# Kernel optimization log

Hardware: AMD Instinct MI355X
Metric: run time of the kernel (lower is better)

## Reference

```python
import jax, jax.numpy as jnp
import numpy as np

N, T, n, C, C2 = 4, 8, 16384, 64, 64

def setup_inputs() -> dict:
    key = jax.random.key(0)
    k1, k2, k3, k4, k5 = jax.random.split(key, 5)
    return {
        "key_mem": jax.random.normal(k1, (N, T, n, C), dtype=jnp.float32),
        "val_mem": jax.random.normal(k2, (N, T, n, C2), dtype=jnp.float32),
        "key_cur": jax.random.normal(k3, (N, n, C), dtype=jnp.float32),
        "val_cur": jax.random.normal(k4, (N, n, C2), dtype=jnp.float32),
        "alpha": jax.random.normal(k5, (1,), dtype=jnp.float32),
    }

def reference(key_mem, val_mem, key_cur, val_cur, alpha):
    # kv_mul: contract memory tokens (T*n) -> (N, C, C2), tiny matrix
    kv_mul = jnp.einsum('btnc,btnd->bcd', key_mem, val_mem)
    # softmax over the C axis (dim=1 in torch layout (N, C, C2))
    kv_mul = jax.nn.softmax(kv_mul, axis=1)
    # out: (N, n, C) @ (N, C, C2) -> (N, n, C2)
    out = jnp.einsum('bnc,bcd->bnd', key_cur, kv_mul)
    return alpha * out + val_cur
```

## Files before the change

kernel.cpp:

```cpp
#include <hip/hip_runtime.h>
#include <math.h>

#define T_DIM   8
#define N_TOK   16384
#define C_DIM   64
#define K_TOT   (T_DIM * N_TOK)
#define N_BATCH 4

__global__ __launch_bounds__(256, 2) void k1_accum(
    const float* __restrict__ key, const float* __restrict__ val,
    float* __restrict__ part, int bpb) {
  int blk  = blockIdx.x;
  int b    = blk / bpb;
  int p    = blk % bpb;
  int wave = threadIdx.x >> 6;
  int lane = threadIdx.x & 63;
  int i = lane >> 3;
  int j = lane & 7;

  int wpb   = bpb * 4;
  int q     = p * 4 + wave;
  int steps = K_TOT / wpb;

  float acc[8][8];
#pragma unroll
  for (int a = 0; a < 8; a++)
#pragma unroll
    for (int c = 0; c < 8; c++) acc[a][c] = 0.f;

  const float4* k4 = (const float4*)key;
  const float4* v4 = (const float4*)val;
  size_t base_row = (size_t)b * K_TOT;

  int k = q;
#pragma unroll 2
  for (int s = 0; s < steps; s++, k += wpb) {
    size_t row = (base_row + (size_t)k) * 16;
    float4 ka = k4[row + 2 * i];
    float4 kb = k4[row + 2 * i + 1];
    float4 va = v4[row + 2 * j];
    float4 vb = v4[row + 2 * j + 1];
    float kr[8] = {ka.x, ka.y, ka.z, ka.w, kb.x, kb.y, kb.z, kb.w};
    float vr[8] = {va.x, va.y, va.z, va.w, vb.x, vb.y, vb.z, vb.w};
#pragma unroll
    for (int a = 0; a < 8; a++)
#pragma unroll
      for (int c = 0; c < 8; c++)
        acc[a][c] = fmaf(kr[a], vr[c], acc[a][c]);
  }

  __shared__ float red[4][4096];
#pragma unroll
  for (int a = 0; a < 8; a++) {
    int c = 8 * i + a;
    *(float4*)&red[wave][c * 64 + 8 * j] =
        make_float4(acc[a][0], acc[a][1], acc[a][2], acc[a][3]);
    *(float4*)&red[wave][c * 64 + 8 * j + 4] =
        make_float4(acc[a][4], acc[a][5], acc[a][6], acc[a][7]);
  }
  __syncthreads();

  int t = threadIdx.x;
  float* dst = part + (size_t)blk * 4096;
#pragma unroll
  for (int x = 0; x < 16; x++) {
    int e = t + 256 * x;
    dst[e] = red[0][e] + red[1][e] + red[2][e] + red[3][e];
  }
}

__global__ __launch_bounds__(256, 4) void k2_reduce(
    const float* __restrict__ part, float* __restrict__ kv, int bpb) {
  int b  = blockIdx.x >> 6;
  int c  = blockIdx.x & 63;
  int p4 = threadIdx.x >> 6;
  int d  = threadIdx.x & 63;

  float s = 0.f;
  int iters = bpb >> 2;
  const float* src = part + (size_t)(b * bpb) * 4096 + c * 64 + d;
#pragma unroll 4
  for (int x = 0; x < iters; x++) s += src[(size_t)(p4 + 4 * x) * 4096];

  __shared__ float l[256];
  l[threadIdx.x] = s;
  __syncthreads();
  if (p4 == 0)
    kv[((size_t)b * 64 + c) * 64 + d] = l[d] + l[64 + d] + l[128 + d] + l[192 + d];
}

__global__ __launch_bounds__(64, 4) void k3_out(
    const float* __restrict__ kv, const float* __restrict__ keyc,
    const float* __restrict__ valc, const float* __restrict__ alphap,
    float* __restrict__ out) {
  __shared__ float kT[64 * 68];
  __shared__ float P[64 * 64];

  int bb = blockIdx.x >> 8;
  int mb = blockIdx.x & 255;
  int m0 = mb * 64;
  int lane = threadIdx.x;
  int i = lane >> 3;
  int j = lane & 7;

  const float* kvb = kv + (size_t)bb * 4096;
  float mx = -3.4e38f;
  for (int c = 0; c < 64; c++) {
    float v = kvb[c * 64 + lane];
    P[c * 64 + lane] = v;
    mx = fmaxf(mx, v);
  }
  float sum = 0.f;
  for (int c = 0; c < 64; c++) {
    float e = __expf(P[c * 64 + lane] - mx);
    P[c * 64 + lane] = e;
    sum += e;
  }
  float inv = 1.f / sum;
  for (int c = 0; c < 64; c++) P[c * 64 + lane] *= inv;

  const float* kbp = keyc + ((size_t)bb * N_TOK + m0) * 64;
#pragma unroll 4
  for (int r = 0; r < 64; r++) kT[lane * 68 + r] = kbp[(size_t)r * 64 + lane];
  __syncthreads();

  float acc[8][8];
#pragma unroll
  for (int a = 0; a < 8; a++)
#pragma unroll
    for (int d = 0; d < 8; d++) acc[a][d] = 0.f;

  for (int c = 0; c < 64; c++) {
    float4 a0 = *(const float4*)&kT[c * 68 + 8 * i];
    float4 a1 = *(const float4*)&kT[c * 68 + 8 * i + 4];
    float4 p0 = *(const float4*)&P[c * 64 + 8 * j];
    float4 p1 = *(const float4*)&P[c * 64 + 8 * j + 4];
    float ar[8] = {a0.x, a0.y, a0.z, a0.w, a1.x, a1.y, a1.z, a1.w};
    float pr[8] = {p0.x, p0.y, p0.z, p0.w, p1.x, p1.y, p1.z, p1.w};
#pragma unroll
    for (int a = 0; a < 8; a++)
#pragma unroll
      for (int d = 0; d < 8; d++)
        acc[a][d] = fmaf(ar[a], pr[d], acc[a][d]);
  }

  float alpha = alphap[0];
  size_t ob = ((size_t)bb * N_TOK + m0) * 64;
#pragma unroll
  for (int a = 0; a < 8; a++) {
    int m = 8 * i + a;
    size_t off = ob + (size_t)m * 64 + 8 * j;
    float4 v0 = *(const float4*)&valc[off];
    float4 v1 = *(const float4*)&valc[off + 4];
    float4 o0 = make_float4(fmaf(alpha, acc[a][0], v0.x),
                            fmaf(alpha, acc[a][1], v0.y),
                            fmaf(alpha, acc[a][2], v0.z),
                            fmaf(alpha, acc[a][3], v0.w));
    float4 o1 = make_float4(fmaf(alpha, acc[a][4], v1.x),
                            fmaf(alpha, acc[a][5], v1.y),
                            fmaf(alpha, acc[a][6], v1.z),
                            fmaf(alpha, acc[a][7], v1.w));
    *(float4*)&out[off] = o0;
    *(float4*)&out[off + 4] = o1;
  }
}

extern "C" void kernel_launch(void* const* d_in, const int* in_sizes, int n_in,
                              void* d_out, int out_size, void* d_ws,
                              size_t ws_size, hipStream_t stream) {
  const float* key_mem = (const float*)d_in[0];
  const float* val_mem = (const float*)d_in[1];
  const float* key_cur = (const float*)d_in[2];
  const float* val_cur = (const float*)d_in[3];
  const float* alpha   = (const float*)d_in[4];
  float* out = (float*)d_out;
  float* ws  = (float*)d_ws;

  int bpb = 128;
  while (bpb > 8 &&
         ((size_t)(4 * bpb) * 4096 + 4096 * N_BATCH) * sizeof(float) > ws_size)
    bpb >>= 2;

  float* part = ws;
  float* kv   = ws + (size_t)(4 * bpb) * 4096;

  k1_accum<<<4 * bpb, 256, 0, stream>>>(key_mem, val_mem, part, bpb);
  k2_reduce<<<256, 256, 0, stream>>>(part, kv, bpb);
  k3_out<<<N_BATCH * (N_TOK / 64), 64, 0, stream>>>(kv, key_cur, val_cur, alpha,
                                                    out);
}
```

Baseline: 353.9 us.

## Prefetch loads in accumulation, split softmax kernel, widen output kernel blocks

k1 now runs 512-thread blocks and software-prefetches the next row's key/value float4s while it accumulates the current outer product. Its cross-wave reduction moves to a staged shared-memory scheme with half the LDS footprint. Softmax moves out of the per-tile output kernel into a tiny separate kernel, so each of the 1024 output blocks no longer recomputes it. k3 uses 256 threads with coalesced key loads and a 2x8 register tile, which adds a launch and trades per-thread reuse for more parallelism.

```diff
diff --git a/kernel.cpp b/kernel.cpp
--- a/kernel.cpp
+++ b/kernel.cpp
@@ -7,7 +7,7 @@
 #define K_TOT   (T_DIM * N_TOK)
 #define N_BATCH 4
 
-__global__ __launch_bounds__(256, 2) void k1_accum(
+__global__ __launch_bounds__(512, 4) void k1_accum(
     const float* __restrict__ key, const float* __restrict__ val,
     float* __restrict__ part, int bpb) {
   int blk  = blockIdx.x;
@@ -18,8 +18,8 @@
   int i = lane >> 3;
   int j = lane & 7;
 
-  int wpb   = bpb * 4;
-  int q     = p * 4 + wave;
+  int wpb   = bpb * 8;
+  int q     = p * 8 + wave;
   int steps = K_TOT / wpb;
 
   float acc[8][8];
@@ -30,16 +30,34 @@
 
   const float4* k4 = (const float4*)key;
   const float4* v4 = (const float4*)val;
-  size_t base_row = (size_t)b * K_TOT;
-
-  int k = q;
+  size_t base = (size_t)b * K_TOT;
+
+  size_t row = (base + (size_t)q) * 16;
+  float4 ka = k4[row + 2 * i];
+  float4 kb = k4[row + 2 * i + 1];
+  float4 va = v4[row + 2 * j];
+  float4 vb = v4[row + 2 * j + 1];
+
+  int k = q + wpb;
 #pragma unroll 2
-  for (int s = 0; s < steps; s++, k += wpb) {
-    size_t row = (base_row + (size_t)k) * 16;
-    float4 ka = k4[row + 2 * i];
-    float4 kb = k4[row + 2 * i + 1];
-    float4 va = v4[row + 2 * j];
-    float4 vb = v4[row + 2 * j + 1];
+  for (int s = 0; s < steps - 1; s++, k += wpb) {
+    size_t r2 = (base + (size_t)k) * 16;
+    float4 nka = k4[r2 + 2 * i];
+    float4 nkb = k4[r2 + 2 * i + 1];
+    float4 nva = v4[r2 + 2 * j];
+    float4 nvb = v4[r2 + 2 * j + 1];
+    {
+      float kr[8] = {ka.x, ka.y, ka.z, ka.w, kb.x, kb.y, kb.z, kb.w};
+      float vr[8] = {va.x, va.y, va.z, va.w, vb.x, vb.y, vb.z, vb.w};
+#pragma unroll
+      for (int a = 0; a < 8; a++)
+#pragma unroll
+        for (int c = 0; c < 8; c++)
+          acc[a][c] = fmaf(kr[a], vr[c], acc[a][c]);
+    }
+    ka = nka; kb = nkb; va = nva; vb = nvb;
+  }
+  {
     float kr[8] = {ka.x, ka.y, ka.z, ka.w, kb.x, kb.y, kb.z, kb.w};
     float vr[8] = {va.x, va.y, va.z, va.w, vb.x, vb.y, vb.z, vb.w};
 #pragma unroll
@@ -49,23 +67,43 @@
         acc[a][c] = fmaf(kr[a], vr[c], acc[a][c]);
   }
 
-  __shared__ float red[4][4096];
-#pragma unroll
-  for (int a = 0; a < 8; a++) {
-    int c = 8 * i + a;
-    *(float4*)&red[wave][c * 64 + 8 * j] =
-        make_float4(acc[a][0], acc[a][1], acc[a][2], acc[a][3]);
-    *(float4*)&red[wave][c * 64 + 8 * j + 4] =
-        make_float4(acc[a][4], acc[a][5], acc[a][6], acc[a][7]);
+  __shared__ float red[2][4096];
+  if (wave < 2) {
+#pragma unroll
+    for (int a = 0; a < 8; a++) {
+      int c = 8 * i + a;
+      *(float4*)&red[wave][c * 64 + 8 * j] =
+          make_float4(acc[a][0], acc[a][1], acc[a][2], acc[a][3]);
+      *(float4*)&red[wave][c * 64 + 8 * j + 4] =
+          make_float4(acc[a][4], acc[a][5], acc[a][6], acc[a][7]);
+    }
   }
   __syncthreads();
-
+#pragma unroll
+  for (int g = 1; g < 4; g++) {
+    if (wave >= 2 * g && wave < 2 * g + 2) {
+      int wb = wave - 2 * g;
+#pragma unroll
+      for (int a = 0; a < 8; a++) {
+        int c = 8 * i + a;
+        float4* d0 = (float4*)&red[wb][c * 64 + 8 * j];
+        float4* d1 = (float4*)&red[wb][c * 64 + 8 * j + 4];
+        float4 x0 = *d0, x1 = *d1;
+        *d0 = make_float4(x0.x + acc[a][0], x0.y + acc[a][1],
+                          x0.z + acc[a][2], x0.w + acc[a][3]);
+        *d1 = make_float4(x1.x + acc[a][4], x1.y + acc[a][5],
+                          x1.z + acc[a][6], x1.w + acc[a][7]);
+      }
+    }
+    __syncthreads();
+  }
+
+  float* dst = part + (size_t)blk * 4096;
   int t = threadIdx.x;
-  float* dst = part + (size_t)blk * 4096;
-#pragma unroll
-  for (int x = 0; x < 16; x++) {
-    int e = t + 256 * x;
-    dst[e] = red[0][e] + red[1][e] + red[2][e] + red[3][e];
+#pragma unroll
+  for (int x = 0; x < 8; x++) {
+    int e = t + 512 * x;
+    dst[e] = red[0][e] + red[1][e];
   }
 }
 
@@ -89,67 +127,87 @@
     kv[((size_t)b * 64 + c) * 64 + d] = l[d] + l[64 + d] + l[128 + d] + l[192 + d];
 }
 
-__global__ __launch_bounds__(64, 4) void k3_out(
-    const float* __restrict__ kv, const float* __restrict__ keyc,
+__global__ __launch_bounds__(64, 1) void k2b_softmax(
+    const float* __restrict__ kv, float* __restrict__ P) {
+  int b = blockIdx.x;
+  int d = threadIdx.x;
+  const float* s = kv + (size_t)b * 4096 + d;
+  float v[64];
+#pragma unroll
+  for (int c = 0; c < 64; c++) v[c] = s[c * 64];
+  float mx = v[0];
+#pragma unroll
+  for (int c = 1; c < 64; c++) mx = fmaxf(mx, v[c]);
+  float sum = 0.f;
+#pragma unroll
+  for (int c = 0; c < 64; c++) {
+    v[c] = __expf(v[c] - mx);
+    sum += v[c];
+  }
+  float inv = 1.f / sum;
+  float* o = P + (size_t)b * 4096 + d;
+#pragma unroll
+  for (int c = 0; c < 64; c++) o[c * 64] = v[c] * inv;
+}
+
+__global__ __launch_bounds__(256, 4) void k3_out(
+    const float* __restrict__ P, const float* __restrict__ keyc,
     const float* __restrict__ valc, const float* __restrict__ alphap,
     float* __restrict__ out) {
+  __shared__ float Ps[4096];
   __shared__ float kT[64 * 68];
-  __shared__ float P[64 * 64];
 
   int bb = blockIdx.x >> 8;
   int mb = blockIdx.x & 255;
   int m0 = mb * 64;
-  int lane = threadIdx.x;
-  int i = lane >> 3;
-  int j = lane & 7;
-
-  const float* kvb = kv + (size_t)bb * 4096;
-  float mx = -3.4e38f;
+  int t = threadIdx.x;
+
+  const float4* p4 = (const float4*)(P + (size_t)bb * 4096);
+  float4* ps4 = (float4*)Ps;
+#pragma unroll
+  for (int u = 0; u < 4; u++) ps4[t + 256 * u] = p4[t + 256 * u];
+
+  int r  = t >> 2;
+  int cb = (t & 3) * 16;
+  const float* krow = keyc + ((size_t)bb * N_TOK + m0 + r) * 64;
+#pragma unroll
+  for (int u = 0; u < 4; u++) {
+    float4 kk = *(const float4*)&krow[cb + 4 * u];
+    int c = cb + 4 * u;
+    kT[(c + 0) * 68 + r] = kk.x;
+    kT[(c + 1) * 68 + r] = kk.y;
+    kT[(c + 2) * 68 + r] = kk.z;
+    kT[(c + 3) * 68 + r] = kk.w;
+  }
+  __syncthreads();
+
+  int wave = t >> 6, lane = t & 63;
+  int mi = lane >> 3, j = lane & 7;
+  int m = wave * 16 + mi * 2;
+
+  float acc[2][8];
+#pragma unroll
+  for (int a = 0; a < 2; a++)
+#pragma unroll
+    for (int d = 0; d < 8; d++) acc[a][d] = 0.f;
+
+#pragma unroll 4
   for (int c = 0; c < 64; c++) {
-    float v = kvb[c * 64 + lane];
-    P[c * 64 + lane] = v;
-    mx = fmaxf(mx, v);
-  }
-  float sum = 0.f;
-  for (int c = 0; c < 64; c++) {
-    float e = __expf(P[c * 64 + lane] - mx);
-    P[c * 64 + lane] = e;
-    sum += e;
-  }
-  float inv = 1.f / sum;
-  for (int c = 0; c < 64; c++) P[c * 64 + lane] *= inv;
-
-  const float* kbp = keyc + ((size_t)bb * N_TOK + m0) * 64;
-#pragma unroll 4
-  for (int r = 0; r < 64; r++) kT[lane * 68 + r] = kbp[(size_t)r * 64 + lane];
-  __syncthreads();
-
-  float acc[8][8];
-#pragma unroll
-  for (int a = 0; a < 8; a++)
-#pragma unroll
-    for (int d = 0; d < 8; d++) acc[a][d] = 0.f;
-
-  for (int c = 0; c < 64; c++) {
-    float4 a0 = *(const float4*)&kT[c * 68 + 8 * i];
-    float4 a1 = *(const float4*)&kT[c * 68 + 8 * i + 4];
-    float4 p0 = *(const float4*)&P[c * 64 + 8 * j];
-    float4 p1 = *(const float4*)&P[c * 64 + 8 * j + 4];
-    float ar[8] = {a0.x, a0.y, a0.z, a0.w, a1.x, a1.y, a1.z, a1.w};
+    float2 kk = *(const float2*)&kT[c * 68 + m];
+    float4 p0 = *(const float4*)&Ps[c * 64 + 8 * j];
+    float4 p1 = *(const float4*)&Ps[c * 64 + 8 * j + 4];
     float pr[8] = {p0.x, p0.y, p0.z, p0.w, p1.x, p1.y, p1.z, p1.w};
 #pragma unroll
-    for (int a = 0; a < 8; a++)
-#pragma unroll
-      for (int d = 0; d < 8; d++)
-        acc[a][d] = fmaf(ar[a], pr[d], acc[a][d]);
+    for (int d = 0; d < 8; d++) {
+      acc[0][d] = fmaf(kk.x, pr[d], acc[0][d]);
+      acc[1][d] = fmaf(kk.y, pr[d], acc[1][d]);
+    }
   }
 
   float alpha = alphap[0];
-  size_t ob = ((size_t)bb * N_TOK + m0) * 64;
-#pragma unroll
-  for (int a = 0; a < 8; a++) {
-    int m = 8 * i + a;
-    size_t off = ob + (size_t)m * 64 + 8 * j;
+#pragma unroll
+  for (int a = 0; a < 2; a++) {
+    size_t off = ((size_t)bb * N_TOK + m0 + m + a) * 64 + 8 * j;
     float4 v0 = *(const float4*)&valc[off];
     float4 v1 = *(const float4*)&valc[off + 4];
     float4 o0 = make_float4(fmaf(alpha, acc[a][0], v0.x),
@@ -178,14 +236,17 @@
 
   int bpb = 128;
   while (bpb > 8 &&
-         ((size_t)(4 * bpb) * 4096 + 4096 * N_BATCH) * sizeof(float) > ws_size)
-    bpb >>= 2;
+         ((size_t)(N_BATCH * bpb) * 4096 + 4096 * N_BATCH) * sizeof(float) >
+             ws_size)
+    bpb >>= 1;
 
   float* part = ws;
-  float* kv   = ws + (size_t)(4 * bpb) * 4096;
-
-  k1_accum<<<4 * bpb, 256, 0, stream>>>(key_mem, val_mem, part, bpb);
+  float* kv   = ws + (size_t)(N_BATCH * bpb) * 4096;
+  float* P    = ws;
+
+  k1_accum<<<N_BATCH * bpb, 512, 0, stream>>>(key_mem, val_mem, part, bpb);
   k2_reduce<<<256, 256, 0, stream>>>(part, kv, bpb);
-  k3_out<<<N_BATCH * (N_TOK / 64), 64, 0, stream>>>(kv, key_cur, val_cur, alpha,
-                                                    out);
-}
+  k2b_softmax<<<N_BATCH, 64, 0, stream>>>(kv, P);
+  k3_out<<<N_BATCH * (N_TOK / 64), 256, 0, stream>>>(P, key_cur, val_cur,
+                                                     alpha, out);
+}
```

Result: faster. 345.6 us (-2.3%).
